# Kernel tuning notes

Hardware: AMD Instinct MI355X
Metric: run time of the kernel (lower is better)

The kernel has to match this reference:

```python
import jax, jax.numpy as jnp
import numpy as np

B, S, D, H, DH = 2, 2048, 768, 12, 64
ROT, BASE, WIN = 64, 10000.0, 128
SCALE = float(np.sqrt(DH))  # cfg.attn_scale = sqrt(d_head) = 8.0


def _sin_cos():
    # TransformerLens calculate_sin_cos_rotary, rotary_adjacent_pairs=False
    pos = jnp.arange(S, dtype=jnp.float32)
    freq = BASE ** (jnp.arange(0, ROT, 2, dtype=jnp.float32) / ROT)
    freq = jnp.concatenate([freq, freq])  # 'd -> (2 d)'
    angles = pos[:, None] / freq[None, :]  # [S, ROT]
    return jnp.sin(angles), jnp.cos(angles)


def _rotate_every_two(v):
    n = v.shape[-1] // 2
    return jnp.concatenate([-v[..., n:], v[..., :n]], axis=-1)


def _apply_rotary(x, sin, cos):
    # x: [B, S, H, DH]; rotate first ROT dims, pass rest through
    xr, xp = x[..., :ROT], x[..., ROT:]
    c = cos[None, :, None, :]
    s = sin[None, :, None, :]
    return jnp.concatenate([xr * c + _rotate_every_two(xr) * s, xp], axis=-1)


def setup_inputs() -> dict:
    key = jax.random.key(0)
    ks = jax.random.split(key, 7)
    init = lambda k, shape: jax.random.normal(k, shape, jnp.float32) / np.sqrt(D).astype(np.float32)
    return dict(
        query_input=jax.random.normal(ks[0], (B, S, D), jnp.float32),
        key_input=jax.random.normal(ks[1], (B, S, D), jnp.float32),
        value_input=jax.random.normal(ks[2], (B, S, D), jnp.float32),
        W_Q=init(ks[3], (H, D, DH)),
        W_K=init(ks[4], (H, D, DH)),
        W_V=init(ks[5], (H, D, DH)),
        W_O=init(ks[6], (H, DH, D)),
        b_Q=jnp.zeros((H, DH), jnp.float32),
        b_K=jnp.zeros((H, DH), jnp.float32),
        b_V=jnp.zeros((H, DH), jnp.float32),
        b_O=jnp.zeros((D,), jnp.float32),
    )


def reference(query_input, key_input, value_input, W_Q, W_K, W_V, W_O, b_Q, b_K, b_V, b_O):
    # QKV projections (calculate_qkv_matrices)
    q = jnp.einsum('bpd,hdk->bphk', query_input, W_Q) + b_Q
    k = jnp.einsum('bpd,hdk->bphk', key_input, W_K) + b_K
    v = jnp.einsum('bpd,hdk->bphk', value_input, W_V) + b_V
    # rotary (kv_cache_pos_offset = 0)
    sin, cos = _sin_cos()
    q = _apply_rotary(q, sin, cos)
    k = _apply_rotary(k, sin, cos)
    # attention scores
    scores = jnp.einsum('bqhd,bkhd->bhqk', q, k) / SCALE
    # position_bias defaults to zeros -> no-op
    i = jnp.arange(S)[:, None]
    j = jnp.arange(S)[None, :]
    mask = (j <= i) & (j > i - WIN)
    scores = jnp.where(mask[None, None], scores, -jnp.inf)
    pattern = jax.nn.softmax(scores, axis=-1)
    pattern = jnp.where(jnp.isnan(pattern), 0.0, pattern)
    z = jnp.einsum('bhqk,bkhd->bqhd', pattern, v)  # [B, S, H, DH]
    # output projection: z flattened @ W_O (rearranged) + b_O
    out = z.reshape(B, S, H * DH) @ W_O.reshape(H * DH, D) + b_O
    return out
```

## Files before the change

### kernel.cpp

```cpp
#include <hip/hip_runtime.h>
#include <hip/hip_bf16.h>

#define BB 2
#define SS 2048
#define DD 768
#define HH 12
#define DHH 64
#define WIN 128
#define MM (BB*SS)

typedef __attribute__((ext_vector_type(8))) short bfrag;
typedef __attribute__((ext_vector_type(4))) float f32x4;
typedef __attribute__((ext_vector_type(4))) short s16x4;

#define AS3(p) ((__attribute__((address_space(3))) void*)(p))
#define AS1(p) ((const __attribute__((address_space(1))) void*)(p))

__device__ inline unsigned short f2bf(float f) {
    union { __hip_bfloat16 h; unsigned short u; } cv;
    cv.h = __float2bfloat16(f);
    return cv.u;
}

__device__ inline void stage128(unsigned short* dst, const unsigned short* src,
                                int w4, int l) {
    #pragma unroll
    for (int j = 0; j < 2; j++) {
        int eoff = (w4 * 2 + j) * 512;
        int e = eoff + l * 8;
        int row = e >> 5;
        int k8 = ((e >> 3) & 3) ^ ((row >> 1) & 3);
        __builtin_amdgcn_global_load_lds(AS1(src + (size_t)row * DD + k8 * 8),
                                         AS3(dst + eoff), 16, 0, 0);
    }
}
__device__ inline void stage64(unsigned short* dst, const unsigned short* src,
                               int w4, int l) {
    int eoff = w4 * 512;
    int e = eoff + l * 8;
    int row = e >> 5;
    int k8 = ((e >> 3) & 3) ^ ((row >> 1) & 3);
    __builtin_amdgcn_global_load_lds(AS1(src + (size_t)row * DD + k8 * 8),
                                     AS3(dst + eoff), 16, 0, 0);
}

__global__ __launch_bounds__(256) void pack_kernel(
    const float* __restrict__ Xq, const float* __restrict__ Xk, const float* __restrict__ Xv,
    const float* __restrict__ Wq, const float* __restrict__ Wk, const float* __restrict__ Wv,
    const float* __restrict__ Wo,
    unsigned short* __restrict__ Wt, unsigned short* __restrict__ Wot,
    float2* __restrict__ rope, unsigned short* __restrict__ Xbf)
{
    __shared__ float T[64][65];
    const int bid = blockIdx.x, t = threadIdx.x;
    if (bid < 432) {
        int proj = bid / 144, rem = bid % 144;
        int h = rem / 12, d0 = (rem % 12) * 64;
        const float* src = (proj == 0 ? Wq : (proj == 1 ? Wk : Wv)) + (size_t)h * DD * DHH;
        int row = t >> 2, c0 = (t & 3) * 16;
        const float4* p4 = reinterpret_cast<const float4*>(src + (size_t)(d0 + row) * DHH + c0);
        float4 x0 = p4[0], x1 = p4[1], x2 = p4[2], x3 = p4[3];
        float* tr = &T[row][c0];
        tr[0]=x0.x; tr[1]=x0.y; tr[2]=x0.z; tr[3]=x0.w;
        tr[4]=x1.x; tr[5]=x1.y; tr[6]=x1.z; tr[7]=x1.w;
        tr[8]=x2.x; tr[9]=x2.y; tr[10]=x2.z; tr[11]=x2.w;
        tr[12]=x3.x; tr[13]=x3.y; tr[14]=x3.z; tr[15]=x3.w;
        __syncthreads();
        int dh = t >> 2;
        unsigned short tmp[16];
        #pragma unroll
        for (int j = 0; j < 16; j++) tmp[j] = f2bf(T[c0 + j][dh]);
        unsigned short* dst = Wt + (size_t)proj * DD * DD + (size_t)(h * 64 + dh) * DD + d0 + c0;
        *reinterpret_cast<bfrag*>(dst)     = *reinterpret_cast<bfrag*>(tmp);
        *reinterpret_cast<bfrag*>(dst + 8) = *reinterpret_cast<bfrag*>(tmp + 8);
    } else if (bid < 576) {
        int id2 = bid - 432;
        int k0 = (id2 / 12) * 64, n0 = (id2 % 12) * 64;
        int row = t >> 2, c0 = (t & 3) * 16;
        const float4* p4 = reinterpret_cast<const float4*>(Wo + (size_t)(k0 + row) * DD + n0 + c0);
        float4 x0 = p4[0], x1 = p4[1], x2 = p4[2], x3 = p4[3];
        float* tr = &T[row][c0];
        tr[0]=x0.x; tr[1]=x0.y; tr[2]=x0.z; tr[3]=x0.w;
        tr[4]=x1.x; tr[5]=x1.y; tr[6]=x1.z; tr[7]=x1.w;
        tr[8]=x2.x; tr[9]=x2.y; tr[10]=x2.z; tr[11]=x2.w;
        tr[12]=x3.x; tr[13]=x3.y; tr[14]=x3.z; tr[15]=x3.w;
        __syncthreads();
        int nr = t >> 2;
        unsigned short tmp[16];
        #pragma unroll
        for (int j = 0; j < 16; j++) tmp[j] = f2bf(T[c0 + j][nr]);
        unsigned short* dst = Wot + (size_t)(n0 + nr) * DD + k0 + c0;
        *reinterpret_cast<bfrag*>(dst)     = *reinterpret_cast<bfrag*>(tmp);
        *reinterpret_cast<bfrag*>(dst + 8) = *reinterpret_cast<bfrag*>(tmp + 8);
    } else if (bid < 832) {
        int idx = (bid - 576) * 256 + t;
        int p = idx >> 5, i2 = idx & 31;
        float inv_freq = exp2f(-(float)i2 * (13.287712379549449f / 32.0f));
        float s, c;
        sincosf((float)p * inv_freq, &s, &c);
        rope[idx] = make_float2(s, c);
    } else {
        int i = bid - 832;
        int proj = i / 768;
        size_t off = (size_t)(i % 768) * 4096 + t * 16;
        const float* src = (proj == 0 ? Xq : (proj == 1 ? Xk : Xv)) + off;
        const float4* p4 = reinterpret_cast<const float4*>(src);
        float4 a0 = p4[0], a1 = p4[1], a2 = p4[2], a3 = p4[3];
        unsigned short u[16];
        u[0]=f2bf(a0.x); u[1]=f2bf(a0.y); u[2]=f2bf(a0.z); u[3]=f2bf(a0.w);
        u[4]=f2bf(a1.x); u[5]=f2bf(a1.y); u[6]=f2bf(a1.z); u[7]=f2bf(a1.w);
        u[8]=f2bf(a2.x); u[9]=f2bf(a2.y); u[10]=f2bf(a2.z); u[11]=f2bf(a2.w);
        u[12]=f2bf(a3.x); u[13]=f2bf(a3.y); u[14]=f2bf(a3.z); u[15]=f2bf(a3.w);
        unsigned short* dst = Xbf + (size_t)proj * MM * DD + off;
        *reinterpret_cast<bfrag*>(dst)     = *reinterpret_cast<bfrag*>(u);
        *reinterpret_cast<bfrag*>(dst + 8) = *reinterpret_cast<bfrag*>(u + 8);
    }
}

__global__ __launch_bounds__(256) void qkv_gemm_kernel(
    const unsigned short* __restrict__ Xbf,
    const unsigned short* __restrict__ Wt,
    const float* __restrict__ bq, const float* __restrict__ bk, const float* __restrict__ bv,
    const float2* __restrict__ rope,
    unsigned short* __restrict__ qo, unsigned short* __restrict__ ko, unsigned short* __restrict__ vo)
{
    const int mt0  = blockIdx.x * 128;
    const int n0   = blockIdx.y * 128;
    const int proj = blockIdx.z;
    const unsigned short* X = Xbf + (size_t)proj * MM * DD + (size_t)mt0 * DD;
    const unsigned short* W = Wt + (size_t)proj * DD * DD + (size_t)n0 * DD;
    const float* bias = proj == 0 ? bq : (proj == 1 ? bk : bv);

    __shared__ unsigned short smem[3 * 8192];

    const int t = threadIdx.x;
    const int l = t & 63, w4 = t >> 6;
    const int l16 = l & 15, quad = l >> 4;
    const int wr = w4 >> 1, wc = w4 & 1;
    const int swz = (l16 >> 1) & 3;

    f32x4 acc[16] = {};

    stage128(smem,               X,      w4, l);
    stage128(smem + 4096,        W,      w4, l);
    stage128(smem + 8192,        X + 32, w4, l);
    stage128(smem + 8192 + 4096, W + 32, w4, l);

    for (int it = 0; it < 24; ++it) {
        unsigned short* Ac = smem + (it % 3) * 8192;
        unsigned short* Bc = Ac + 4096;
        if (it < 23) asm volatile("s_waitcnt vmcnt(4)" ::: "memory");
        else         asm volatile("s_waitcnt vmcnt(0)" ::: "memory");
        __builtin_amdgcn_s_barrier();
        if (it < 22) {
            unsigned short* An = smem + ((it + 2) % 3) * 8192;
            stage128(An,        X + (it + 2) * 32, w4, l);
            stage128(An + 4096, W + (it + 2) * 32, w4, l);
        }
        bfrag af[4], bg[4];
        #pragma unroll
        for (int mi = 0; mi < 4; mi++)
            af[mi] = *reinterpret_cast<const bfrag*>(&Ac[(wr * 64 + mi * 16 + l16) * 32 + ((quad ^ swz) * 8)]);
        #pragma unroll
        for (int ni = 0; ni < 4; ni++)
            bg[ni] = *reinterpret_cast<const bfrag*>(&Bc[(wc * 64 + ni * 16 + l16) * 32 + ((quad ^ swz) * 8)]);
        #pragma unroll
        for (int mi = 0; mi < 4; mi++)
            #pragma unroll
            for (int ni = 0; ni < 4; ni++)
                acc[mi * 4 + ni] = __builtin_amdgcn_mfma_f32_16x16x32_bf16(af[mi], bg[ni], acc[mi * 4 + ni], 0, 0, 0);
    }
    __syncthreads();

    unsigned short* Ct = smem;
    const int b = mt0 >> 11;
    if (proj < 2) {
        #pragma unroll
        for (int ni = 0; ni < 4; ni++) {
            int nloc = wc * 64 + ni * 16 + l16;
            int n = n0 + nloc;
            int dh = n & 63;
            float bv0 = bias[n];
            float bv1 = bias[n ^ 32];
            float sgn = (dh & 32) ? 1.0f : -1.0f;
            const float2* rp = rope + (dh & 31);
            #pragma unroll
            for (int mi = 0; mi < 4; mi++)
                #pragma unroll
                for (int r = 0; r < 4; r++) {
                    int ploc = wr * 64 + mi * 16 + quad * 4 + r;
                    int p = (mt0 + ploc) & (SS - 1);
                    float2 sc = rp[p << 5];
                    float val = acc[mi * 4 + ni][r] + bv0;
                    float pr  = acc[mi * 4 + (ni ^ 2)][r] + bv1;
                    Ct[ploc * 140 + nloc] = f2bf(val * sc.y + sgn * pr * sc.x);
                }
        }
        __syncthreads();
        unsigned short* dst = (proj == 0) ? qo : ko;
        #pragma unroll
        for (int jj = 0; jj < 8; jj++) {
            int id = jj * 256 + t;
            int row = id >> 4, c = (id & 15) * 8;
            int n = n0 + c, h = n >> 6, dh = n & 63;
            int p = (mt0 + row) & (SS - 1);
            bfrag vv = *reinterpret_cast<const bfrag*>(&Ct[row * 140 + c]);
            *reinterpret_cast<bfrag*>(dst + (((size_t)(b * HH + h) * SS + p) << 6) + dh) = vv;
        }
    } else {
        #pragma unroll
        for (int ni = 0; ni < 4; ni++) {
            int nloc = wc * 64 + ni * 16 + l16;
            float bv0 = bias[n0 + nloc];
            #pragma unroll
            for (int mi = 0; mi < 4; mi++)
                #pragma unroll
                for (int r = 0; r < 4; r++) {
                    int ploc = wr * 64 + mi * 16 + quad * 4 + r;
                    Ct[nloc * 140 + ploc] = f2bf(acc[mi * 4 + ni][r] + bv0);
                }
        }
        __syncthreads();
        int p0 = mt0 & (SS - 1);
        #pragma unroll
        for (int jj = 0; jj < 8; jj++) {
            int id = jj * 256 + t;
            int row = id >> 4, c = (id & 15) * 8;
            int n = n0 + row, h = n >> 6, dh = n & 63;
            bfrag vv = *reinterpret_cast<const bfrag*>(&Ct[row * 140 + c]);
            *reinterpret_cast<bfrag*>(vo + (((size_t)(b * HH + h) * DHH + dh) << 11) + p0 + c) = vv;
        }
    }
}

__global__ __launch_bounds__(256) void attn_kernel(
    const unsigned short* __restrict__ q,
    const unsigned short* __restrict__ k,
    const unsigned short* __restrict__ v,
    unsigned short* __restrict__ z)
{
    const int qb = blockIdx.x * 64;
    const int h  = blockIdx.y;
    const int b  = blockIdx.z;
    const int kb = qb - WIN;

    __shared__ unsigned short sA[25088];

    const int t = threadIdx.x;
    const int w4 = t >> 6, l = t & 63;
    const int l16 = l & 15, quad = l >> 4;
    const int swz = (l16 >> 1) & 3;

    const size_t qkbase = (size_t)(b * HH + h) * SS * DHH;
    const unsigned short* kp = (k + qkbase) + (ptrdiff_t)kb * DHH;
    const unsigned short* vp = (v + (size_t)(b * HH + h) * DHH * SS) + (ptrdiff_t)kb;

    #pragma unroll
    for (int j = 0; j < 6; j++) {
        int g = w4 * 6 + j;
        int panel = g >> 2, sub = g & 3;
        int rg = panel >> 1, kpart = panel & 1;
        int e = sub * 512 + l * 8;
        int row = e >> 5;
        int k8 = ((e >> 3) & 3) ^ ((row >> 1) & 3);
        __builtin_amdgcn_global_load_lds(
            AS1(kp + (size_t)(rg * 64 + row) * DHH + kpart * 32 + k8 * 8),
            AS3(sA + panel * 2048 + sub * 512), 16, 0, 0);
    }
    #pragma unroll
    for (int j = 0; j < 6; j++) {
        int g = w4 * 6 + j;
        int F = g * 64 + l;
        int d = F / 24, s = F % 24;
        int cs = s ^ (d & 7);
        __builtin_amdgcn_global_load_lds(
            AS1(vp + (size_t)d * SS + cs * 8),
            AS3(sA + 12800 + g * 512), 16, 0, 0);
    }
    bfrag qf[2];
    #pragma unroll
    for (int kk = 0; kk < 2; kk++)
        qf[kk] = *reinterpret_cast<const bfrag*>(
            q + qkbase + (size_t)(qb + 16 * w4 + l16) * DHH + kk * 32 + quad * 8);

    __syncthreads();

    f32x4 sacc[12] = {};
    #pragma unroll
    for (int kk = 0; kk < 2; kk++)
        #pragma unroll
        for (int mt = 0; mt < 12; mt++) {
            int kr = 16 * mt + l16;
            bfrag bf = *reinterpret_cast<const bfrag*>(
                &sA[(((kr >> 6) * 2 + kk) * 2048) + (kr & 63) * 32 + ((quad ^ swz) * 8)]);
            sacc[mt] = __builtin_amdgcn_mfma_f32_16x16x32_bf16(qf[kk], bf, sacc[mt], 0, 0, 0);
        }

    float mx[4] = {-3e38f, -3e38f, -3e38f, -3e38f};
    #pragma unroll
    for (int mt = 0; mt < 12; mt++)
        #pragma unroll
        for (int r = 0; r < 4; r++) {
            int row = 16 * w4 + quad * 4 + r;
            int c = 16 * mt + l16;
            bool valid = (c > row) && (c <= row + WIN) && (kb + c >= 0);
            float s = valid ? sacc[mt][r] * 0.125f : -3e38f;
            sacc[mt][r] = s;
            mx[r] = fmaxf(mx[r], s);
        }
    #pragma unroll
    for (int off = 1; off < 16; off <<= 1)
        #pragma unroll
        for (int r = 0; r < 4; r++) mx[r] = fmaxf(mx[r], __shfl_xor(mx[r], off, 64));
    float sum[4] = {0.f, 0.f, 0.f, 0.f};
    #pragma unroll
    for (int mt = 0; mt < 12; mt++)
        #pragma unroll
        for (int r = 0; r < 4; r++) {
            float p = __expf(sacc[mt][r] - mx[r]);
            sacc[mt][r] = p;
            sum[r] += p;
        }
    #pragma unroll
    for (int off = 1; off < 16; off <<= 1)
        #pragma unroll
        for (int r = 0; r < 4; r++) sum[r] += __shfl_xor(sum[r], off, 64);
    float inv[4];
    #pragma unroll
    for (int r = 0; r < 4; r++) inv[r] = 1.0f / sum[r];

    __syncthreads();

    unsigned short* Ps = sA;
    #pragma unroll
    for (int mt = 0; mt < 12; mt++)
        #pragma unroll
        for (int r = 0; r < 4; r++)
            Ps[(16 * w4 + quad * 4 + r) * 200 + 16 * mt + l16] = f2bf(sacc[mt][r] * inv[r]);

    unsigned short* Vt = sA + 12800;
    f32x4 zacc[4] = {};
    #pragma unroll
    for (int ci = 0; ci < 6; ci++) {
        bfrag pb = *reinterpret_cast<const bfrag*>(
            &Ps[(16 * w4 + l16) * 200 + ci * 32 + quad * 8]);
        #pragma unroll
        for (int mt = 0; mt < 4; mt++) {
            int d = 16 * mt + l16;
            bfrag va = *reinterpret_cast<const bfrag*>(
                &Vt[d * 192 + (((ci * 4 + quad) ^ (l16 & 7)) * 8)]);
            zacc[mt] = __builtin_amdgcn_mfma_f32_16x16x32_bf16(va, pb, zacc[mt], 0, 0, 0);
        }
    }
    size_t zrow = ((size_t)(b * SS + qb + 16 * w4 + l16)) * (HH * DHH) + h * DHH;
    #pragma unroll
    for (int mt = 0; mt < 4; mt++) {
        s16x4 pk;
        pk[0] = (short)f2bf(zacc[mt][0]);
        pk[1] = (short)f2bf(zacc[mt][1]);
        pk[2] = (short)f2bf(zacc[mt][2]);
        pk[3] = (short)f2bf(zacc[mt][3]);
        *reinterpret_cast<s16x4*>(z + zrow + 16 * mt + quad * 4) = pk;
    }
}

__global__ __launch_bounds__(256) void out_gemm_kernel(
    const unsigned short* __restrict__ Z,
    const unsigned short* __restrict__ Wot,
    const float* __restrict__ bo,
    float* __restrict__ out)
{
    const int mt0 = blockIdx.x * 64;
    const int n0  = blockIdx.y * 64;
    const unsigned short* A = Z + (size_t)mt0 * DD;
    const unsigned short* Bw = Wot + (size_t)n0 * DD;

    __shared__ unsigned short smem[4 * 4096];

    const int t = threadIdx.x;
    const int l = t & 63, w4 = t >> 6;
    const int l16 = l & 15, quad = l >> 4;
    const int swz = (l16 >> 1) & 3;

    f32x4 acc[4] = {};

    stage64(smem,               A,       w4, l);
    stage64(smem + 2048,        Bw,      w4, l);
    stage64(smem + 4096,        A  + 32, w4, l);
    stage64(smem + 4096 + 2048, Bw + 32, w4, l);
    stage64(smem + 8192,        A  + 64, w4, l);
    stage64(smem + 8192 + 2048, Bw + 64, w4, l);

    for (int it = 0; it < 24; ++it) {
        unsigned short* Ac = smem + (it & 3) * 4096;
        unsigned short* Bc = Ac + 2048;
        if (it < 22)       asm volatile("s_waitcnt vmcnt(4)" ::: "memory");
        else if (it == 22) asm volatile("s_waitcnt vmcnt(2)" ::: "memory");
        else               asm volatile("s_waitcnt vmcnt(0)" ::: "memory");
        __builtin_amdgcn_s_barrier();
        if (it < 21) {
            unsigned short* An = smem + ((it + 3) & 3) * 4096;
            stage64(An,        A  + (it + 3) * 32, w4, l);
            stage64(An + 2048, Bw + (it + 3) * 32, w4, l);
        }
        bfrag af = *reinterpret_cast<const bfrag*>(&Ac[(w4 * 16 + l16) * 32 + ((quad ^ swz) * 8)]);
        #pragma unroll
        for (int ni = 0; ni < 4; ni++) {
            bfrag bg = *reinterpret_cast<const bfrag*>(&Bc[(ni * 16 + l16) * 32 + ((quad ^ swz) * 8)]);
            acc[ni] = __builtin_amdgcn_mfma_f32_16x16x32_bf16(af, bg, acc[ni], 0, 0, 0);
        }
    }

    #pragma unroll
    for (int ni = 0; ni < 4; ni++) {
        int n = n0 + ni * 16 + l16;
        float bv0 = bo[n];
        #pragma unroll
        for (int r = 0; r < 4; r++) {
            int m = mt0 + w4 * 16 + quad * 4 + r;
            out[(size_t)m * DD + n] = acc[ni][r] + bv0;
        }
    }
}

extern "C" void kernel_launch(void* const* d_in, const int* in_sizes, int n_in,
                              void* d_out, int out_size, void* d_ws, size_t ws_size,
                              hipStream_t stream) {
    const float* Xq = (const float*)d_in[0];
    const float* Xk = (const float*)d_in[1];
    const float* Xv = (const float*)d_in[2];
    const float* Wq = (const float*)d_in[3];
    const float* Wk = (const float*)d_in[4];
    const float* Wv = (const float*)d_in[5];
    const float* Wo = (const float*)d_in[6];
    const float* bq = (const float*)d_in[7];
    const float* bk = (const float*)d_in[8];
    const float* bv = (const float*)d_in[9];
    const float* bo = (const float*)d_in[10];
    float* out = (float*)d_out;

    const size_t seg = (size_t)BB * HH * SS * DHH;
    unsigned short* q   = (unsigned short*)d_ws;
    unsigned short* k   = q + seg;
    unsigned short* v   = k + seg;
    unsigned short* z   = v + seg;
    unsigned short* Wt  = z + seg;
    unsigned short* Wot = Wt + (size_t)3 * DD * DD;
    float2* rope = (float2*)(Wot + (size_t)DD * DD);
    unsigned short* Xbf = (unsigned short*)(rope + 2048 * 32);

    pack_kernel<<<dim3(3136), 256, 0, stream>>>(Xq, Xk, Xv, Wq, Wk, Wv, Wo, Wt, Wot, rope, Xbf);
    qkv_gemm_kernel<<<dim3(MM / 128, DD / 128, 3), 256, 0, stream>>>(
        Xbf, Wt, bq, bk, bv, rope, q, k, v);
    attn_kernel<<<dim3(SS / 64, HH, BB), 256, 0, stream>>>(q, k, v, z);
    out_gemm_kernel<<<dim3(MM / 64, DD / 64), 256, 0, stream>>>(z, Wot, bo, out);
}
```

Baseline: 165.3 us.

## Skip fully masked score tiles per wave and deepen out-GEMM K-steps

In the attention kernel each wave now computes only the 9 key tiles that can intersect its 16-row band of the sliding window, not all 12. It zeroes one extra P tile so the PV loop can run 5 chunks starting at a wave-dependent offset, and it raises wave priority around the MFMA loops with s_setprio. The output GEMM switches from a 4-stage pipeline of 32-wide K slices to a 3-stage pipeline of 64-wide slices, halving the number of barriers. The result depends on the per-wave tile offsets and the zero padding exactly covering the window.

```diff
diff --git a/kernel.cpp b/kernel.cpp
--- a/kernel.cpp
+++ b/kernel.cpp
@@ -285,27 +285,29 @@
 
     __syncthreads();
 
-    f32x4 sacc[12] = {};
+    f32x4 sacc[9] = {};
+    __builtin_amdgcn_s_setprio(1);
     #pragma unroll
     for (int kk = 0; kk < 2; kk++)
         #pragma unroll
-        for (int mt = 0; mt < 12; mt++) {
-            int kr = 16 * mt + l16;
+        for (int j = 0; j < 9; j++) {
+            int kr = 16 * (w4 + j) + l16;
             bfrag bf = *reinterpret_cast<const bfrag*>(
                 &sA[(((kr >> 6) * 2 + kk) * 2048) + (kr & 63) * 32 + ((quad ^ swz) * 8)]);
-            sacc[mt] = __builtin_amdgcn_mfma_f32_16x16x32_bf16(qf[kk], bf, sacc[mt], 0, 0, 0);
-        }
+            sacc[j] = __builtin_amdgcn_mfma_f32_16x16x32_bf16(qf[kk], bf, sacc[j], 0, 0, 0);
+        }
+    __builtin_amdgcn_s_setprio(0);
 
     float mx[4] = {-3e38f, -3e38f, -3e38f, -3e38f};
     #pragma unroll
-    for (int mt = 0; mt < 12; mt++)
+    for (int j = 0; j < 9; j++)
         #pragma unroll
         for (int r = 0; r < 4; r++) {
             int row = 16 * w4 + quad * 4 + r;
-            int c = 16 * mt + l16;
+            int c = 16 * (w4 + j) + l16;
             bool valid = (c > row) && (c <= row + WIN) && (kb + c >= 0);
-            float s = valid ? sacc[mt][r] * 0.125f : -3e38f;
-            sacc[mt][r] = s;
+            float s = valid ? sacc[j][r] * 0.125f : -3e38f;
+            sacc[j][r] = s;
             mx[r] = fmaxf(mx[r], s);
         }
     #pragma unroll
@@ -314,11 +316,11 @@
         for (int r = 0; r < 4; r++) mx[r] = fmaxf(mx[r], __shfl_xor(mx[r], off, 64));
     float sum[4] = {0.f, 0.f, 0.f, 0.f};
     #pragma unroll
-    for (int mt = 0; mt < 12; mt++)
+    for (int j = 0; j < 9; j++)
         #pragma unroll
         for (int r = 0; r < 4; r++) {
-            float p = __expf(sacc[mt][r] - mx[r]);
-            sacc[mt][r] = p;
+            float p = __expf(sacc[j][r] - mx[r]);
+            sacc[j][r] = p;
             sum[r] += p;
         }
     #pragma unroll
@@ -333,15 +335,23 @@
 
     unsigned short* Ps = sA;
     #pragma unroll
-    for (int mt = 0; mt < 12; mt++)
+    for (int j = 0; j < 9; j++)
         #pragma unroll
         for (int r = 0; r < 4; r++)
-            Ps[(16 * w4 + quad * 4 + r) * 200 + 16 * mt + l16] = f2bf(sacc[mt][r] * inv[r]);
+            Ps[(16 * w4 + quad * 4 + r) * 200 + 16 * (w4 + j) + l16] = f2bf(sacc[j][r] * inv[r]);
+    {
+        int mtz = (w4 & 1) ? (w4 - 1) : (w4 + 9);
+        #pragma unroll
+        for (int r = 0; r < 4; r++)
+            Ps[(16 * w4 + quad * 4 + r) * 200 + 16 * mtz + l16] = 0;
+    }
 
     unsigned short* Vt = sA + 12800;
     f32x4 zacc[4] = {};
-    #pragma unroll
-    for (int ci = 0; ci < 6; ci++) {
+    __builtin_amdgcn_s_setprio(1);
+    #pragma unroll
+    for (int ji = 0; ji < 5; ji++) {
+        int ci = (w4 >> 1) + ji;
         bfrag pb = *reinterpret_cast<const bfrag*>(
             &Ps[(16 * w4 + l16) * 200 + ci * 32 + quad * 8]);
         #pragma unroll
@@ -352,6 +362,7 @@
             zacc[mt] = __builtin_amdgcn_mfma_f32_16x16x32_bf16(va, pb, zacc[mt], 0, 0, 0);
         }
     }
+    __builtin_amdgcn_s_setprio(0);
     size_t zrow = ((size_t)(b * SS + qb + 16 * w4 + l16)) * (HH * DHH) + h * DHH;
     #pragma unroll
     for (int mt = 0; mt < 4; mt++) {
@@ -375,7 +386,7 @@
     const unsigned short* A = Z + (size_t)mt0 * DD;
     const unsigned short* Bw = Wot + (size_t)n0 * DD;
 
-    __shared__ unsigned short smem[4 * 4096];
+    __shared__ unsigned short smem[3 * 8192];
 
     const int t = threadIdx.x;
     const int l = t & 63, w4 = t >> 6;
@@ -384,30 +395,38 @@
 
     f32x4 acc[4] = {};
 
-    stage64(smem,               A,       w4, l);
-    stage64(smem + 2048,        Bw,      w4, l);
-    stage64(smem + 4096,        A  + 32, w4, l);
-    stage64(smem + 4096 + 2048, Bw + 32, w4, l);
-    stage64(smem + 8192,        A  + 64, w4, l);
-    stage64(smem + 8192 + 2048, Bw + 64, w4, l);
-
-    for (int it = 0; it < 24; ++it) {
-        unsigned short* Ac = smem + (it & 3) * 4096;
-        unsigned short* Bc = Ac + 2048;
-        if (it < 22)       asm volatile("s_waitcnt vmcnt(4)" ::: "memory");
-        else if (it == 22) asm volatile("s_waitcnt vmcnt(2)" ::: "memory");
-        else               asm volatile("s_waitcnt vmcnt(0)" ::: "memory");
+    #pragma unroll
+    for (int s = 0; s < 2; s++) {
+        unsigned short* sl = smem + s * 8192;
+        stage64(sl,        A  + s * 64,      w4, l);
+        stage64(sl + 2048, A  + s * 64 + 32, w4, l);
+        stage64(sl + 4096, Bw + s * 64,      w4, l);
+        stage64(sl + 6144, Bw + s * 64 + 32, w4, l);
+    }
+
+    for (int it = 0; it < 12; ++it) {
+        unsigned short* Ac = smem + (it % 3) * 8192;
+        unsigned short* Bc = Ac + 4096;
+        if (it < 11) asm volatile("s_waitcnt vmcnt(4)" ::: "memory");
+        else         asm volatile("s_waitcnt vmcnt(0)" ::: "memory");
         __builtin_amdgcn_s_barrier();
-        if (it < 21) {
-            unsigned short* An = smem + ((it + 3) & 3) * 4096;
-            stage64(An,        A  + (it + 3) * 32, w4, l);
-            stage64(An + 2048, Bw + (it + 3) * 32, w4, l);
-        }
-        bfrag af = *reinterpret_cast<const bfrag*>(&Ac[(w4 * 16 + l16) * 32 + ((quad ^ swz) * 8)]);
-        #pragma unroll
-        for (int ni = 0; ni < 4; ni++) {
-            bfrag bg = *reinterpret_cast<const bfrag*>(&Bc[(ni * 16 + l16) * 32 + ((quad ^ swz) * 8)]);
-            acc[ni] = __builtin_amdgcn_mfma_f32_16x16x32_bf16(af, bg, acc[ni], 0, 0, 0);
+        if (it < 10) {
+            unsigned short* An = smem + ((it + 2) % 3) * 8192;
+            stage64(An,        A  + (it + 2) * 64,      w4, l);
+            stage64(An + 2048, A  + (it + 2) * 64 + 32, w4, l);
+            stage64(An + 4096, Bw + (it + 2) * 64,      w4, l);
+            stage64(An + 6144, Bw + (it + 2) * 64 + 32, w4, l);
+        }
+        #pragma unroll
+        for (int kk = 0; kk < 2; kk++) {
+            bfrag af = *reinterpret_cast<const bfrag*>(
+                &Ac[kk * 2048 + (w4 * 16 + l16) * 32 + ((quad ^ swz) * 8)]);
+            #pragma unroll
+            for (int ni = 0; ni < 4; ni++) {
+                bfrag bg = *reinterpret_cast<const bfrag*>(
+                    &Bc[kk * 2048 + (ni * 16 + l16) * 32 + ((quad ^ swz) * 8)]);
+                acc[ni] = __builtin_amdgcn_mfma_f32_16x16x32_bf16(af, bg, acc[ni], 0, 0, 0);
+            }
         }
     }
 
```

Result: no change. 162.6 us (-1.6%).
